# Optimization experiments

Hardware: AMD Instinct MI355X
Metric: run time of the kernel (lower is better)

Reference implementation:

```python
import jax, jax.numpy as jnp
import numpy as np

B, L, D, H = 4, 2048, 256, 512


def silu_backward(x):
    s = jax.nn.silu(x)
    return s + jax.nn.sigmoid(x) * (1.0 - s)


def setup_inputs() -> dict:
    key = jax.random.key(0)
    ks = jax.random.split(key, 12)
    sc = 0.02
    return {
        "x": jax.random.normal(ks[0], (B, L, D), jnp.float32),
        "W1": jax.random.normal(ks[1], (B, H, D), jnp.float32) * sc,
        "W2": jax.random.normal(ks[2], (B, D, H), jnp.float32) * sc,
        "Wq": jax.random.normal(ks[3], (D, D), jnp.float32) * sc,
        "bq": jnp.zeros((D,), jnp.float32),
        "Wk": jax.random.normal(ks[4], (D, D), jnp.float32) * sc,
        "bk": jnp.zeros((D,), jnp.float32),
        "Wv": jax.random.normal(ks[5], (D, D), jnp.float32) * sc,
        "bv": jnp.zeros((D,), jnp.float32),
        "w_lr": jax.random.normal(ks[6], (D,), jnp.float32) * sc,
        "b_lr": jnp.zeros((), jnp.float32),
        "w_wd": jax.random.normal(ks[7], (D,), jnp.float32) * sc,
        "b_wd": jnp.zeros((), jnp.float32),
        "log_base_lr": jnp.asarray(np.log(0.1), jnp.float32),
        "log_base_wd": jnp.asarray(np.log(0.5), jnp.float32),
    }


def reference(x, W1, W2, Wq, bq, Wk, bk, Wv, bv, w_lr, b_lr, w_wd, b_wd, log_base_lr, log_base_wd):
    b, l, d = x.shape
    query = x @ Wq + bq
    key = x @ Wk + bk
    value = x @ Wv + bv
    lr = jnp.exp(log_base_lr) * jax.nn.sigmoid(x @ w_lr + b_lr)          # [b,l]
    log_wd = jnp.log(1.0 - jnp.exp(log_base_wd) * jax.nn.sigmoid(x @ w_wd + b_wd))  # [b,l]

    wd_cross = jnp.exp(jnp.cumsum(log_wd, axis=1))                       # [b,l]
    idx = jnp.arange(l)
    strict_upper = idx[:, None] < idx[None, :]                           # (m, j): j > m
    A = jnp.where(strict_upper[None], log_wd[:, None, :], 0.0)           # [b,m,j]
    wd_inner = jnp.exp(jnp.cumsum(A, axis=2)) * (idx[:, None] <= idx[None, :])[None]  # [b,m,j]

    X1 = key
    Z1 = jnp.einsum('bhd,bld->blh', W1, X1)
    X2 = jax.nn.silu(Z1)
    Z2 = jnp.einsum('bdh,blh->bld', W2, X2)
    grad_Z2 = Z2 - value
    grad_X2 = jnp.einsum('bdh,bld->blh', W2, grad_Z2)
    grad_Z1 = silu_backward(Z1) * grad_X2

    X1_ = query
    mask_X1X1_ = jnp.einsum('bld,bmd->blm', X1, X1_) * wd_inner
    Z1_inner = -jnp.einsum('blh,bl,blm->bmh', grad_Z1, lr, mask_X1X1_)
    Z1_cross = jnp.einsum('bhd,bld,bl->blh', W1, X1_, wd_cross)
    Z1_ = Z1_inner + Z1_cross

    W1_next = (-jnp.einsum('blh,bl,bld->bhd', grad_Z1, lr * wd_inner[:, :, -1], X1)
               + W1 * wd_cross[:, -1][:, None, None])

    X2_ = jax.nn.silu(Z1_)
    mask_X2X2_ = jnp.einsum('blh,bmh->blm', X2, X2_) * wd_inner
    Z2_inner = -jnp.einsum('bld,bl,blm->bmd', grad_Z2, lr, mask_X2X2_)
    Z2_cross = jnp.einsum('bdh,blh,bl->bld', W2, X2_, wd_cross)
    Z2_ = Z2_inner + Z2_cross

    W2_next = (-jnp.einsum('bld,bl,blh->bdh', grad_Z2, lr * wd_inner[:, :, -1], X2)
               + W2 * wd_cross[:, -1][:, None, None])

    return (Z2_, W1_next, W2_next)
```

## Files before the change

kernel.cpp:

```cpp
#include <hip/hip_runtime.h>

typedef __bf16 bf16;
typedef __bf16 bf16x8 __attribute__((ext_vector_type(8)));
typedef __bf16 bf16x4 __attribute__((ext_vector_type(4)));
typedef float  f32x4  __attribute__((ext_vector_type(4)));

#define SB 72
#define CUTOFF -18.0

__device__ __forceinline__ float silu_f(float x){
  float s = 1.f/(1.f+__expf(-x));
  return x*s;
}
__device__ __forceinline__ float silu_bwd_f(float x){
  float s = 1.f/(1.f+__expf(-x));
  float si = x*s;
  return si + s*(1.f-si);
}

struct MArgs {
  const bf16* A; const bf16* B;
  long sA, sB;
  int lda, ldb;
  int M, N, K;
  int mode;
  float* Cf; long sCf;
  bf16*  Cb; long sCb;
  bf16*  Cb2; long sCb2;
  bf16*  Ct;  long sCt;  int ldct;
  bf16*  Ct2; long sCt2;
  int ldc;
  const float* auxf; int ldax; long sAuxf;
  const bf16*  auxb; long sAuxb;
  const float* rowv; long sRowv;
  const float* rowv2; long sRowv2;
  const double* cd;  long sCd;
  const float* clp;  long sClp;
  bf16* Q; bf16* Ko; float* Vo; const float* bqkv;
};

template<int TM>
__device__ __forceinline__ void gemm_body(const MArgs& g, int bm, int bn, int bz)
{
  constexpr int TTP = (TM==64) ? 72 : 136;
  constexpr int BUF = (TM+64)*SB;
  __shared__ __align__(16) bf16 sh[2*BUF];

  const int row0 = bm*TM, col0 = bn*64;
  constexpr int NI  = TM/32;
  constexpr int TPR = 256/TM;
  constexpr int EPR = 64/TPR;
  constexpr int NCH = EPR/8;

  const bf16* A = g.A + (long)bz*g.sA;
  const bf16* B = g.B + (long)bz*g.sB;
  const double* cd = g.cd ? g.cd + (long)bz*g.sCd : (const double*)0;
  float* Cf = g.Cf ? g.Cf + (long)bz*g.sCf : (float*)0;
  bf16* Cb  = g.Cb ? g.Cb + (long)bz*g.sCb : (bf16*)0;
  bf16* Cb2 = g.Cb2 ? g.Cb2 + (long)bz*g.sCb2 : (bf16*)0;
  bf16* Ct  = g.Ct ? g.Ct + (long)bz*g.sCt : (bf16*)0;
  bf16* Ct2 = g.Ct2 ? g.Ct2 + (long)bz*g.sCt2 : (bf16*)0;
  const float* auxf = g.auxf ? g.auxf + (long)bz*g.sAuxf : (const float*)0;
  const bf16*  auxb = g.auxb ? g.auxb + (long)bz*g.sAuxb : (const bf16*)0;
  const float* rowv = g.rowv ? g.rowv + (long)bz*g.sRowv : (const float*)0;
  const float* rowv2 = g.rowv2 ? g.rowv2 + (long)bz*g.sRowv2 : (const float*)0;

  const int tid = threadIdx.x;
  const int mode = g.mode;
  const int lane = tid & 63;
  const int w = tid >> 6;
  const int wr = (w >> 1) * (TM/2), wc = (w & 1) * 32;
  const int l15 = lane & 15;
  const int quad = lane >> 4;

  f32x4 acc[NI][2];
  #pragma unroll
  for (int i=0;i<NI;i++)
    #pragma unroll
    for (int j=0;j<2;j++)
      #pragma unroll
      for (int r=0;r<4;r++) acc[i][j][r] = 0.f;

  const int rowA = tid / TPR, kA = (tid % TPR) * EPR;
  const int rowB = tid >> 2,  kB = (tid & 3) * 16;

  int klo = 0;
  if (cd && mode == 10) {
    const double cref = cd[g.K-1];
    const int nch = g.K >> 6;
    bool dead = (lane < nch-1) && ((cref - cd[lane*64+63]) < CUTOFF);
    unsigned long long mask = __ballot(dead);
    klo = (int)__builtin_ctzll(~mask) * 64;
  }

  const bf16* Abase = A + (long)(row0+rowA)*g.lda + kA;
  const bf16* Bbase = B + (long)(col0+rowB)*g.ldb + kB;

  bf16x8 paA[NCH], pbA0, pbA1, paB[NCH], pbB0, pbB1;
  #pragma unroll
  for (int p=0;p<NCH;p++) paA[p] = *(const bf16x8*)(Abase + klo + p*8);
  pbA0 = *(const bf16x8*)(Bbase + klo);
  pbA1 = *(const bf16x8*)(Bbase + klo + 8);
  if (klo + 64 < g.K) {
    #pragma unroll
    for (int p=0;p<NCH;p++) paB[p] = *(const bf16x8*)(Abase + klo + 64 + p*8);
    pbB0 = *(const bf16x8*)(Bbase + klo + 64);
    pbB1 = *(const bf16x8*)(Bbase + klo + 64 + 8);
  }

  auto compute = [&](const bf16* As, const bf16* Bs){
    #pragma unroll
    for (int ch=0; ch<2; ch++){
      bf16x8 af[NI], bf2[2];
      #pragma unroll
      for (int i=0;i<NI;i++) af[i]  = *(const bf16x8*)&As[(wr + i*16 + l15)*SB + ch*32 + quad*8];
      #pragma unroll
      for (int j=0;j<2;j++) bf2[j] = *(const bf16x8*)&Bs[(wc + j*16 + l15)*SB + ch*32 + quad*8];
      #pragma unroll
      for (int i=0;i<NI;i++)
        #pragma unroll
        for (int j=0;j<2;j++)
          acc[i][j] = __builtin_amdgcn_mfma_f32_16x16x32_bf16(af[i], bf2[j], acc[i][j], 0, 0, 0);
    }
  };

  for (int k0 = klo; k0 < g.K; k0 += 128) {
    {
      bf16* As = sh; bf16* Bs = sh + TM*SB;
      #pragma unroll
      for (int p=0;p<NCH;p++) *(bf16x8*)&As[rowA*SB + kA + p*8] = paA[p];
      *(bf16x8*)&Bs[rowB*SB + kB]     = pbA0;
      *(bf16x8*)&Bs[rowB*SB + kB + 8] = pbA1;
      __syncthreads();
      if (k0 + 128 < g.K) {
        #pragma unroll
        for (int p=0;p<NCH;p++) paA[p] = *(const bf16x8*)(Abase + k0 + 128 + p*8);
        pbA0 = *(const bf16x8*)(Bbase + k0 + 128);
        pbA1 = *(const bf16x8*)(Bbase + k0 + 128 + 8);
      }
      compute(As, Bs);
    }
    if (k0 + 64 < g.K) {
      bf16* As = sh + BUF; bf16* Bs = sh + BUF + TM*SB;
      #pragma unroll
      for (int p=0;p<NCH;p++) *(bf16x8*)&As[rowA*SB + kA + p*8] = paB[p];
      *(bf16x8*)&Bs[rowB*SB + kB]     = pbB0;
      *(bf16x8*)&Bs[rowB*SB + kB + 8] = pbB1;
      __syncthreads();
      if (k0 + 192 < g.K) {
        #pragma unroll
        for (int p=0;p<NCH;p++) paB[p] = *(const bf16x8*)(Abase + k0 + 192 + p*8);
        pbB0 = *(const bf16x8*)(Bbase + k0 + 192);
        pbB1 = *(const bf16x8*)(Bbase + k0 + 192 + 8);
      }
      compute(As, Bs);
    }
  }

  float clv = 0.f;
  if (mode == 10) clv = *(g.clp + (long)bz*g.sClp);

  bf16* Pt12 = (bf16*)0; int slotl0 = 0;
  if (mode == 12) {
    const int d = (row0 & ~127) - col0;
    const int slot = (d + 64) >> 7;
    slotl0 = (row0 & ~127) - slot*128;
    Pt12 = Cb + ((long)bm*3 + slot) * (64*128);
  }

  const bool hasT = (TM==64) ? (mode==1 || mode==2 || mode==3)
                             : (mode==11 && col0 >= 256 && col0 < 512);

  #pragma unroll
  for (int i=0;i<NI;i++){
    const int rb = row0 + wr + i*16 + quad*4;
    const int rloc = wr + i*16 + quad*4;
    #pragma unroll
    for (int j=0;j<2;j++){
      const int c = col0 + wc + j*16 + l15;
      const int cloc = wc + j*16 + l15;
      bf16 tv[4], tv2[4]; bool doT = false, doT2 = false;
      #pragma unroll
      for (int reg=0; reg<4; reg++){
        const int r = rb + reg;
        float v = acc[i][j][reg];
        const long co = (long)r*g.ldc + c;
        switch (mode) {
          case 1: {
            Cb[co]  = (bf16)v;
            float sv = silu_f(v);
            Cb2[co] = (bf16)sv;
            tv[reg] = (bf16)(sv * rowv[r]); doT = true;
          } break;
          case 2: {
            bf16 o = (bf16)(v - auxf[(long)r*g.ldax + c]);
            Cb[co] = o; tv[reg] = o; doT = true;
          } break;
          case 3: {
            float v3 = silu_bwd_f((float)auxb[(long)r*g.ldax + c]) * v * rowv[r];
            tv[reg]  = (bf16)v3;
            tv2[reg] = (bf16)(v3 * rowv2[r]);
            doT = true; doT2 = true;
          } break;
          case 10: {
            Cf[co] = v + auxf[(long)r*g.ldax + c]*clv;
          } break;
          case 11: {
            float o = v + g.bqkv[c];
            if (c < 256)      g.Q [(long)r*256 + c]       = (bf16)o;
            else if (c < 512) { g.Ko[(long)r*256 + (c-256)] = (bf16)o; tv[reg] = (bf16)o; doT = true; }
            else              g.Vo[(long)r*256 + (c-512)] = o;
          } break;
          case 12: {
            const float cm = (float)cd[r];
            const float cl = (float)cd[c];
            float pv = -v * __expf(cm - cl);
            if (rowv) pv *= rowv[c];
            if (c > r) pv = 0.f;
            Pt12[(r - row0)*128 + (c - slotl0)] = (bf16)pv;
          } break;
        }
      }
      if (hasT && doT) {
        bf16x4 t4 = { tv[0], tv[1], tv[2], tv[3] };
        *(bf16x4*)&sh[cloc*TTP + rloc] = t4;
        if (doT2) {
          bf16x4 t4b = { tv2[0], tv2[1], tv2[2], tv2[3] };
          *(bf16x4*)&sh[64*72 + cloc*TTP + rloc] = t4b;
        }
      }
    }
  }

  if (hasT) {
    __syncthreads();
    if constexpr (TM == 64) {
      const int cl = tid >> 2, rl = (tid & 3)*16;
      bf16x8 u0 = *(const bf16x8*)&sh[cl*72 + rl];
      bf16x8 u1 = *(const bf16x8*)&sh[cl*72 + rl + 8];
      bf16* d = Ct + (long)(col0+cl)*g.ldct + row0 + rl;
      *(bf16x8*)d       = u0;
      *(bf16x8*)(d + 8) = u1;
      if (mode == 3) {
        bf16x8 v0 = *(const bf16x8*)&sh[64*72 + cl*72 + rl];
        bf16x8 v1 = *(const bf16x8*)&sh[64*72 + cl*72 + rl + 8];
        bf16* d2 = Ct2 + (long)(col0+cl)*g.ldct + row0 + rl;
        *(bf16x8*)d2       = v0;
        *(bf16x8*)(d2 + 8) = v1;
      }
    } else {
      const int cl = tid >> 2, rl = (tid & 3)*32;
      const int b = row0 / g.ldct, l0r = row0 % g.ldct;
      bf16* d = Ct + (long)b*g.sCt + (long)(col0-256+cl)*g.ldct + l0r + rl;
      #pragma unroll
      for (int p=0;p<4;p++)
        *(bf16x8*)(d + p*8) = *(const bf16x8*)&sh[cl*136 + rl + p*8];
    }
  }
}

__device__ __forceinline__ bool pgen_prep(const MArgs& g, int mt, int hs, int bz, int& bnOut)
{
  const int slot = hs >> 1, half = hs & 1;
  const int m0 = mt*64;
  const int l0 = (m0 & ~127) - slot*128;
  if (l0 < 0) return false;
  const double* cd = g.cd + (long)bz*g.sCd;
  const int lref = (l0+127 < m0) ? (l0+127) : m0;
  if (cd[m0] - cd[lref] < CUTOFF) return false;
  const int l0h = l0 + half*64;
  if (l0h > m0) {
    bf16* Pt = g.Cb + (long)bz*g.sCb + ((long)mt*3 + slot) * (64*128);
    const int row = threadIdx.x >> 2, colb = 64 + (threadIdx.x & 3)*16;
    bf16x8 z;
    #pragma unroll
    for (int q=0;q<8;q++) z[q] = (bf16)0.f;
    *(bf16x8*)&Pt[row*128 + colb]     = z;
    *(bf16x8*)&Pt[row*128 + colb + 8] = z;
    return false;
  }
  bnOut = l0h >> 6;
  return true;
}

__global__ __launch_bounds__(256)
void mfma_gemm64(MArgs g){ gemm_body<64>(g, blockIdx.x, blockIdx.y, blockIdx.z); }

struct CumArgs {
  const float* lw; const float* lr;
  double* cd; float* wdc; float* se1; float* se2; int L;
};

__device__ __forceinline__ void cumsum_body(const CumArgs& a, int b)
{
  __shared__ double sum_s[256];
  const int t = threadIdx.x;
  const int L = a.L;
  const float* lwb = a.lw + (long)b*L;
  double loc[8];
  double s = 0.0;
  #pragma unroll
  for (int i=0;i<8;i++){ s += (double)lwb[t*8+i]; loc[i] = s; }
  sum_s[t] = s;
  __syncthreads();
  for (int off=1; off<256; off<<=1){
    double v = 0.0;
    if (t >= off) v = sum_s[t-off];
    __syncthreads();
    sum_s[t] += v;
    __syncthreads();
  }
  const double prefix = (t > 0) ? sum_s[t-1] : 0.0;
  const double total  = sum_s[255];
  #pragma unroll
  for (int i=0;i<8;i++){
    double c = prefix + loc[i];
    long idx = (long)b*L + t*8 + i;
    a.cd[idx]  = c;
    a.wdc[idx] = (float)exp(c);
    double e = exp(total - c);
    a.se1[idx] = (float)(-e);
    a.se2[idx] = (float)(-e) * a.lr[idx];
  }
}


__global__ __launch_bounds__(256)
void qkv_cum(MArgs g, CumArgs c)
{
  if (blockIdx.x == 64) {
    if (blockIdx.y < 4) cumsum_body(c, blockIdx.y);
    return;
  }
  gemm_body<128>(g, blockIdx.x, blockIdx.y, 0);
}

__global__ __launch_bounds__(256)
void gz2p1(MArgs gz, MArgs p1)
{
  const int bid = blockIdx.x;
  if (bid < 512) {
    gemm_body<64>(gz, bid & 31, (bid >> 5) & 3, bid >> 7);
    return;
  }
  const int i = bid - 512;
  const int mt = i & 31, q = i >> 5;
  const int hs = q % 6, bz = q / 6;
  int bn;
  if (pgen_prep(p1, mt, hs, bz, bn))
    gemm_body<64>(p1, mt, bn, bz);
}

__global__ __launch_bounds__(256)
void p2wn(MArgs p2, MArgs w1n, MArgs w2n)
{
  const int bid = blockIdx.x;
  if (bid < 768) {
    const int mt = bid & 31, q = bid >> 5;
    const int hs = q % 6, bz = q / 6;
    int bn;
    if (pgen_prep(p2, mt, hs, bz, bn))
      gemm_body<64>(p2, mt, bn, bz);
    return;
  }
  const int i = bid - 768;
  if (i < 128) {
    gemm_body<64>(w1n, i & 7, (i >> 3) & 3, i >> 5);
    return;
  }
  const int j = i - 128;
  gemm_body<64>(w2n, j & 3, (j >> 2) & 7, j >> 5);
}

struct CArgs {
  const bf16 *A, *W, *P, *B2;
  long sA, sW, sB2;
  int ldb2;
  const double* cd; long sCd;
  const float* wdc; long sWdc;
  float* Cf; long sCf;
  bf16* Cb; long sCb;
  int ldc;
};

template<int KS64, int SILU, int ZSPLIT>
__global__ __launch_bounds__(256)
void cons(CArgs g)
{
  const int mt = blockIdx.x;
  const int m0 = mt*64, n0 = blockIdx.y*64;
  const int bz   = ZSPLIT ? (blockIdx.z >> 1) : blockIdx.z;
  const int half = ZSPLIT ? (blockIdx.z & 1)  : 0;
  const int K1 = KS64*64;
  const bf16* A  = g.A  + (long)bz*g.sA;
  const bf16* W  = g.W  + (long)bz*g.sW;
  const bf16* B2 = g.B2 + (long)bz*g.sB2;
  const double* cd = g.cd + (long)bz*g.sCd;
  const float* wdc = g.wdc + (long)bz*g.sWdc;

  const int tid = threadIdx.x;
  const int lane = tid & 63, w = tid >> 6;
  const int wr = (w>>1)*32, wc = (w&1)*32;
  const int l15 = lane & 15, quad = lane >> 4;
  const int rowA = tid >> 2, kA = (tid & 3) * 16;

  bool alive[3];
  int nalive = 0;
  #pragma unroll
  for (int s=0;s<3;s++){
    const int l0 = (m0 & ~127) - s*128;
    bool a = (l0 >= 0);
    if (a) {
      const int lref = (l0+127 < m0) ? (l0+127) : m0;
      a = (cd[m0] - cd[lref] >= CUTOFF);
    }
    alive[s] = a; nalive += a ? 1 : 0;
  }
  if (ZSPLIT && half == 1 && nalive == 0) return;

  constexpr int BUFC = 128*SB;
  __shared__ __align__(16) bf16 sh[2*BUFC];

  f32x4 O[2][2];
  #pragma unroll
  for (int i=0;i<2;i++)
    #pragma unroll
    for (int j=0;j<2;j++)
      #pragma unroll
      for (int r=0;r<4;r++) O[i][j][r] = 0.f;

  auto compute = [&](const bf16* As, const bf16* Bs){
    #pragma unroll
    for (int ch=0; ch<2; ch++){
      bf16x8 af[2], bfr[2];
      #pragma unroll
      for (int i=0;i<2;i++) af[i]  = *(const bf16x8*)&As[(wr + i*16 + l15)*SB + ch*32 + quad*8];
      #pragma unroll
      for (int j=0;j<2;j++) bfr[j] = *(const bf16x8*)&Bs[(wc + j*16 + l15)*SB + ch*32 + quad*8];
      #pragma unroll
      for (int i=0;i<2;i++)
        #pragma unroll
        for (int j=0;j<2;j++)
          O[i][j] = __builtin_amdgcn_mfma_f32_16x16x32_bf16(af[i], bfr[j], O[i][j], 0, 0, 0);
    }
  };

  if (half == 0) {
    const bf16* Abase = A + (long)(m0+rowA)*K1 + kA;
    const bf16* Wbase = W + (long)(n0+rowA)*K1 + kA;
    bf16x8 aA0,aA1,wA0,wA1, aB0,aB1,wB0,wB1;
    aA0 = *(const bf16x8*)Abase;        aA1 = *(const bf16x8*)(Abase + 8);
    wA0 = *(const bf16x8*)Wbase;        wA1 = *(const bf16x8*)(Wbase + 8);
    aB0 = *(const bf16x8*)(Abase + 64); aB1 = *(const bf16x8*)(Abase + 72);
    wB0 = *(const bf16x8*)(Wbase + 64); wB1 = *(const bf16x8*)(Wbase + 72);
    for (int ks=0; ks<KS64; ks+=2){
      {
        bf16* As = sh; bf16* Bs = sh + 64*SB;
        *(bf16x8*)&As[rowA*SB + kA]     = aA0;
        *(bf16x8*)&As[rowA*SB + kA + 8] = aA1;
        *(bf16x8*)&Bs[rowA*SB + kA]     = wA0;
        *(bf16x8*)&Bs[rowA*SB + kA + 8] = wA1;
        __syncthreads();
        if (ks+2 < KS64) {
          const int kn = (ks+2)*64;
          aA0 = *(const bf16x8*)(Abase + kn); aA1 = *(const bf16x8*)(Abase + kn + 8);
          wA0 = *(const bf16x8*)(Wbase + kn); wA1 = *(const bf16x8*)(Wbase + kn + 8);
        }
        compute(As, Bs);
      }
      {
        bf16* As = sh + BUFC; bf16* Bs = sh + BUFC + 64*SB;
        *(bf16x8*)&As[rowA*SB + kA]     = aB0;
        *(bf16x8*)&As[rowA*SB + kA + 8] = aB1;
        *(bf16x8*)&Bs[rowA*SB + kA]     = wB0;
        *(bf16x8*)&Bs[rowA*SB + kA + 8] = wB1;
        __syncthreads();
        if (ks+3 < KS64) {
          const int kn = (ks+3)*64;
          aB0 = *(const bf16x8*)(Abase + kn); aB1 = *(const bf16x8*)(Abase + kn + 8);
          wB0 = *(const bf16x8*)(Wbase + kn); wB1 = *(const bf16x8*)(Wbase + kn + 8);
        }
        compute(As, Bs);
      }
    }
    #pragma unroll
    for (int i=0;i<2;i++)
      #pragma unroll
      for (int reg=0; reg<4; reg++){
        const float s = wdc[m0 + wr + i*16 + quad*4 + reg];
        #pragma unroll
        for (int j=0;j<2;j++) O[i][j][reg] *= s;
      }
  }

  if (!ZSPLIT || half == 1) {
    int s0a=0, s1a=0, s2a=0, na=0;
    #pragma unroll
    for (int s=0;s<3;s++) if (alive[s]) { if (na==0) s0a=s; else if (na==1) s1a=s; else s2a=s; na++; }
    const int nst = na*2;
    if (nst > 0) {
      auto Pptr = [&](int t)->const bf16* {
        const int i = t>>1;
        const int s = (i==0) ? s0a : ((i==1) ? s1a : s2a);
        return g.P + (((long)bz*32 + mt)*3 + s)*(64*128) + (long)rowA*128 + (t&1)*64 + kA;
      };
      auto Bptr = [&](int t)->const bf16* {
        const int i = t>>1;
        const int s = (i==0) ? s0a : ((i==1) ? s1a : s2a);
        const int l0 = (m0 & ~127) - s*128;
        return B2 + (long)(n0+rowA)*g.ldb2 + l0 + (t&1)*64 + kA;
      };
      bf16x8 pA0,pA1,bA0,bA1, pB0,pB1,bB0,bB1;
      { const bf16* pp = Pptr(0); pA0 = *(const bf16x8*)pp; pA1 = *(const bf16x8*)(pp+8);
        const bf16* bb = Bptr(0); bA0 = *(const bf16x8*)bb; bA1 = *(const bf16x8*)(bb+8); }
      { const bf16* pp = Pptr(1); pB0 = *(const bf16x8*)pp; pB1 = *(const bf16x8*)(pp+8);
        const bf16* bb = Bptr(1); bB0 = *(const bf16x8*)bb; bB1 = *(const bf16x8*)(bb+8); }
      for (int t=0; t<nst; t+=2){
        {
          bf16* As = sh; bf16* Bs = sh + 64*SB;
          *(bf16x8*)&As[rowA*SB + kA]     = pA0;
          *(bf16x8*)&As[rowA*SB + kA + 8] = pA1;
          *(bf16x8*)&Bs[rowA*SB + kA]     = bA0;
          *(bf16x8*)&Bs[rowA*SB + kA + 8] = bA1;
          __syncthreads();
          if (t+2 < nst) {
            const bf16* pp = Pptr(t+2); pA0 = *(const bf16x8*)pp; pA1 = *(const bf16x8*)(pp+8);
            const bf16* bb = Bptr(t+2); bA0 = *(const bf16x8*)bb; bA1 = *(const bf16x8*)(bb+8);
          }
          compute(As, Bs);
        }
        {
          bf16* As = sh + BUFC; bf16* Bs = sh + BUFC + 64*SB;
          *(bf16x8*)&As[rowA*SB + kA]     = pB0;
          *(bf16x8*)&As[rowA*SB + kA + 8] = pB1;
          *(bf16x8*)&Bs[rowA*SB + kA]     = bB0;
          *(bf16x8*)&Bs[rowA*SB + kA + 8] = bB1;
          __syncthreads();
          if (t+3 < nst) {
            const bf16* pp = Pptr(t+3); pB0 = *(const bf16x8*)pp; pB1 = *(const bf16x8*)(pp+8);
            const bf16* bb = Bptr(t+3); bB0 = *(const bf16x8*)bb; bB1 = *(const bf16x8*)(bb+8);
          }
          compute(As, Bs);
        }
      }
    }
  }

  #pragma unroll
  for (int i=0;i<2;i++){
    const int rb = m0 + wr + i*16 + quad*4;
    #pragma unroll
    for (int j=0;j<2;j++){
      const int c = n0 + wc + j*16 + l15;
      #pragma unroll
      for (int reg=0; reg<4; reg++){
        const long co = (long)(rb+reg)*g.ldc + c;
        if (ZSPLIT)     unsafeAtomicAdd(&g.Cf[(long)bz*g.sCf + co], O[i][j][reg]);
        else if (SILU)  g.Cb[(long)bz*g.sCb + co] = (bf16)silu_f(O[i][j][reg]);
        else            g.Cf[(long)bz*g.sCf + co] = O[i][j][reg];
      }
    }
  }
}

struct FrontArgs {
  const float *x, *W1, *W2, *Wq, *Wk, *Wv;
  bf16 *xb, *W1b, *W2b, *Wqkvt, *W2t;
  float* out0;
  const float *wlr, *blr, *wwd, *bwd, *lbl, *lbw;
  float *lr, *lw;
  const float *bq, *bk, *bv; float* bqkv;
  long LD4, HD4, HD;
};

__global__ __launch_bounds__(256)
void front_kernel(FrontArgs f)
{
  __shared__ bf16 t[64][72];
  const int bid = blockIdx.x;
  const int tid = threadIdx.x;

  if (bid < 1536) {
    const float* src; bf16* dst; long n; long base;
    if (bid < 1024)      { src = f.x;  dst = f.xb;  n = f.LD4; base = (long)bid*2048; }
    else if (bid < 1280) { src = f.W1; dst = f.W1b; n = f.HD4; base = (long)(bid-1024)*2048; }
    else                 { src = f.W2; dst = f.W2b; n = f.HD4; base = (long)(bid-1280)*2048; }
    long i = base + (long)tid*8;
    if (i >= n) return;
    float4 a = *(const float4*)&src[i];
    float4 b = *(const float4*)&src[i+4];
    bf16x8 o;
    o[0]=(bf16)a.x; o[1]=(bf16)a.y; o[2]=(bf16)a.z; o[3]=(bf16)a.w;
    o[4]=(bf16)b.x; o[5]=(bf16)b.y; o[6]=(bf16)b.z; o[7]=(bf16)b.w;
    *(bf16x8*)&dst[i] = o;
    return;
  }
  if (bid < 2560) {
    long i = (long)(bid-1536)*2048 + (long)tid*8;
    float4 z = {0.f,0.f,0.f,0.f};
    *(float4*)&f.out0[i]   = z;
    *(float4*)&f.out0[i+4] = z;
    return;
  }
  if (bid < 2736) {
    const float* ip; bf16* op; int R, C; int r0, c0;
    if (bid < 2608) {
      const int r = bid - 2560;
      const int z = r >> 4, rem = r & 15;
      ip = z==0 ? f.Wq : (z==1 ? f.Wk : f.Wv);
      op = f.Wqkvt + (long)z*256*256;
      R = 256; C = 256;
      r0 = (rem & 3)*64; c0 = (rem >> 2)*64;
    } else {
      const int r = bid - 2608;
      const int b = r >> 5, rem = r & 31;
      ip = f.W2 + (long)b*f.HD;
      op = f.W2t + (long)b*f.HD;
      R = 256; C = 512;
      r0 = (rem & 3)*64; c0 = (rem >> 2)*64;
    }
    const int lr_ = tid>>2, lc = (tid&3)*16;
    #pragma unroll
    for (int q=0;q<4;q++){
      float4 a = *(const float4*)&ip[(long)(r0+lr_)*C + c0+lc + q*4];
      t[lr_][lc+q*4+0] = (bf16)a.x; t[lr_][lc+q*4+1] = (bf16)a.y;
      t[lr_][lc+q*4+2] = (bf16)a.z; t[lr_][lc+q*4+3] = (bf16)a.w;
    }
    __syncthreads();
    const int oc = tid>>2, orr = (tid&3)*16;
    bf16x8 u, v;
    #pragma unroll
    for (int i=0;i<8;i++){ u[i] = t[orr+i][oc]; v[i] = t[orr+8+i][oc]; }
    *(bf16x8*)&op[(long)(c0+oc)*R + r0+orr]   = u;
    *(bf16x8*)&op[(long)(c0+oc)*R + r0+orr+8] = v;
    return;
  }
  if (bid < 4784) {
    const int row  = (bid-2736)*4 + (tid >> 6);
    const int lane = tid & 63;
    const float4 a = ((const float4*)(f.x + (long)row*256))[lane];
    const float4 u = ((const float4*)f.wlr)[lane];
    const float4 w = ((const float4*)f.wwd)[lane];
    float d1 = a.x*u.x + a.y*u.y + a.z*u.z + a.w*u.w;
    float d2 = a.x*w.x + a.y*w.y + a.z*w.z + a.w*w.w;
    #pragma unroll
    for (int off=32; off; off>>=1) {
      d1 += __shfl_down(d1, off);
      d2 += __shfl_down(d2, off);
    }
    if (lane == 0) {
      float s1 = 1.f/(1.f+expf(-(d1 + f.blr[0])));
      f.lr[row] = expf(f.lbl[0]) * s1;
      float s2 = 1.f/(1.f+expf(-(d2 + f.bwd[0])));
      f.lw[row] = logf(1.f - expf(f.lbw[0]) * s2);
    }
    return;
  }
  for (int i = tid; i < 768; i += 256)
    f.bqkv[i] = (i<256) ? f.bq[i] : ((i<512) ? f.bk[i-256] : f.bv[i-512]);
}

extern "C" void kernel_launch(void* const* d_in, const int* in_sizes, int n_in,
                              void* d_out, int out_size, void* d_ws, size_t ws_size,
                              hipStream_t stream)
{
  const int Bn = 4, L = 2048, D = 256, H = 512;
  const long LD = (long)L*D, LH = (long)L*H, HD = (long)H*D;

  const float* x   = (const float*)d_in[0];
  const float* W1  = (const float*)d_in[1];
  const float* W2  = (const float*)d_in[2];
  const float* Wq  = (const float*)d_in[3];
  const float* bq  = (const float*)d_in[4];
  const float* Wk  = (const float*)d_in[5];
  const float* bk  = (const float*)d_in[6];
  const float* Wv  = (const float*)d_in[7];
  const float* bv  = (const float*)d_in[8];
  const float* wlr = (const float*)d_in[9];
  const float* blr = (const float*)d_in[10];
  const float* wwd = (const float*)d_in[11];
  const float* bwd = (const float*)d_in[12];
  const float* lbl = (const float*)d_in[13];
  const float* lbw = (const float*)d_in[14];
  (void)in_sizes; (void)n_in; (void)out_size; (void)ws_size;

  float* out0 = (float*)d_out;
  float* out1 = out0 + (long)Bn*LD;
  float* out2 = out1 + (long)Bn*HD;

  char* wsp = (char*)d_ws;
  size_t off = 0;
  auto alloc = [&](size_t bytes)->void*{
    void* p = wsp + off; off += (bytes + 255) & ~(size_t)255; return p;
  };
  bf16* xb    = (bf16*)alloc((size_t)Bn*LD*2);
  bf16* Wqkvt = (bf16*)alloc((size_t)3*D*D*2);
  float* bqkv = (float*)alloc((size_t)3*D*4);
  bf16* W1b  = (bf16*)alloc((size_t)Bn*HD*2);
  bf16* W2b  = (bf16*)alloc((size_t)Bn*HD*2);
  bf16* W2t  = (bf16*)alloc((size_t)Bn*HD*2);
  bf16* Qb   = (bf16*)alloc((size_t)Bn*LD*2);
  bf16* Kb   = (bf16*)alloc((size_t)Bn*LD*2);
  bf16* Kt   = (bf16*)alloc((size_t)Bn*LD*2);
  float* Vf  = (float*)alloc((size_t)Bn*LD*4);
  bf16* Z1b  = (bf16*)alloc((size_t)Bn*LH*2);
  bf16* X2b  = (bf16*)alloc((size_t)Bn*LH*2);
  bf16* X2t  = (bf16*)alloc((size_t)Bn*LH*2);
  bf16* gZb  = (bf16*)alloc((size_t)Bn*LD*2);
  bf16* gZt  = (bf16*)alloc((size_t)Bn*LD*2);
  bf16* A1t  = (bf16*)alloc((size_t)Bn*LH*2);
  bf16* A1s  = (bf16*)alloc((size_t)Bn*LH*2);
  bf16* X2_b = (bf16*)alloc((size_t)Bn*LH*2);
  bf16* Pb1  = (bf16*)alloc((size_t)Bn*32*3*64*128*2);
  bf16* Pb2  = (bf16*)alloc((size_t)Bn*32*3*64*128*2);
  float* lrb = (float*)alloc((size_t)Bn*L*4);
  float* lwb = (float*)alloc((size_t)Bn*L*4);
  float* wdc = (float*)alloc((size_t)Bn*L*4);
  float* se1 = (float*)alloc((size_t)Bn*L*4);
  float* se2 = (float*)alloc((size_t)Bn*L*4);
  double* cdb = (double*)alloc((size_t)Bn*L*8);

  const long sP = (long)32*3*64*128;

  {
    FrontArgs f{};
    f.x = x; f.W1 = W1; f.W2 = W2; f.Wq = Wq; f.Wk = Wk; f.Wv = Wv;
    f.xb = xb; f.W1b = W1b; f.W2b = W2b; f.Wqkvt = Wqkvt; f.W2t = W2t;
    f.out0 = out0;
    f.wlr = wlr; f.blr = blr; f.wwd = wwd; f.bwd = bwd; f.lbl = lbl; f.lbw = lbw;
    f.lr = lrb; f.lw = lwb;
    f.bq = bq; f.bk = bk; f.bv = bv; f.bqkv = bqkv;
    f.LD4 = Bn*LD; f.HD4 = Bn*HD; f.HD = HD;
    front_kernel<<<dim3(4785), 256, 0, stream>>>(f);
  }
  {
    MArgs g{}; g.A = xb; g.lda = D; g.B = Wqkvt; g.ldb = D;
    g.M = Bn*L; g.N = 3*D; g.K = D; g.mode = 11; g.ldc = 0;
    g.Q = Qb; g.Ko = Kb; g.Vo = Vf; g.bqkv = bqkv;
    g.Ct = Kt; g.sCt = LD; g.ldct = L;
    CumArgs ca{ lwb, lrb, cdb, wdc, se1, se2, L };
    qkv_cum<<<dim3(65, 12), 256, 0, stream>>>(g, ca);
  }
  {
    MArgs g{}; g.A = Kb; g.lda = D; g.sA = LD; g.B = W1b; g.ldb = D; g.sB = HD;
    g.M = L; g.N = H; g.K = D; g.mode = 1; g.ldc = H;
    g.Cb = Z1b; g.sCb = LH; g.Cb2 = X2b; g.sCb2 = LH;
    g.Ct = X2t; g.sCt = LH; g.ldct = L;
    g.rowv = se2; g.sRowv = L;
    mfma_gemm64<<<dim3(32, 8, 4), 256, 0, stream>>>(g);
  }
  {
    MArgs gz{}; gz.A = X2b; gz.lda = H; gz.sA = LH; gz.B = W2b; gz.ldb = H; gz.sB = HD;
    gz.M = L; gz.N = D; gz.K = H; gz.mode = 2; gz.ldc = D;
    gz.auxf = Vf; gz.ldax = D; gz.sAuxf = LD; gz.Cb = gZb; gz.sCb = LD;
    gz.Ct = gZt; gz.sCt = LD; gz.ldct = L;

    MArgs p1{}; p1.A = Qb; p1.lda = D; p1.sA = LD; p1.B = Kb; p1.ldb = D; p1.sB = LD;
    p1.K = D; p1.mode = 12; p1.ldc = 0;
    p1.Cb = Pb1; p1.sCb = sP;
    p1.cd = cdb; p1.sCd = L;

    gz2p1<<<dim3(512 + 768), 256, 0, stream>>>(gz, p1);
  }
  {
    MArgs g{}; g.A = gZb; g.lda = D; g.sA = LD; g.B = W2t; g.ldb = D; g.sB = HD;
    g.M = L; g.N = H; g.K = D; g.mode = 3; g.ldc = H;
    g.auxb = Z1b; g.ldax = H; g.sAuxb = LH;
    g.rowv = lrb; g.sRowv = L; g.rowv2 = se1; g.sRowv2 = L;
    g.Ct = A1t; g.sCt = LH; g.ldct = L;
    g.Ct2 = A1s; g.sCt2 = LH;
    mfma_gemm64<<<dim3(32, 8, 4), 256, 0, stream>>>(g);
  }
  {
    CArgs c{};
    c.A = Qb; c.sA = LD; c.W = W1b; c.sW = HD;
    c.P = Pb1; c.B2 = A1t; c.sB2 = LH; c.ldb2 = L;
    c.cd = cdb; c.sCd = L; c.wdc = wdc; c.sWdc = L;
    c.Cb = X2_b; c.sCb = LH; c.ldc = H;
    cons<4,1,0><<<dim3(32, H/64, Bn), 256, 0, stream>>>(c);
  }
  {
    MArgs p2{}; p2.A = X2_b; p2.lda = H; p2.sA = LH; p2.B = X2b; p2.ldb = H; p2.sB = LH;
    p2.K = H; p2.mode = 12; p2.ldc = 0;
    p2.Cb = Pb2; p2.sCb = sP;
    p2.cd = cdb; p2.sCd = L;
    p2.rowv = lrb; p2.sRowv = L;

    MArgs g1{}; g1.A = A1s; g1.lda = L; g1.sA = LH; g1.B = Kt; g1.ldb = L; g1.sB = LD;
    g1.M = H; g1.N = D; g1.K = L; g1.mode = 10; g1.ldc = D;
    g1.cd = cdb; g1.sCd = L;
    g1.auxf = W1; g1.ldax = D; g1.sAuxf = HD; g1.clp = wdc + (L-1); g1.sClp = L;
    g1.Cf = out1; g1.sCf = HD;

    MArgs g2{}; g2.A = gZt; g2.lda = L; g2.sA = LD; g2.B = X2t; g2.ldb = L; g2.sB = LH;
    g2.M = D; g2.N = H; g2.K = L; g2.mode = 10; g2.ldc = H;
    g2.cd = cdb; g2.sCd = L;
    g2.auxf = W2; g2.ldax = H; g2.sAuxf = HD; g2.clp = wdc + (L-1); g2.sClp = L;
    g2.Cf = out2; g2.sCf = HD;

    p2wn<<<dim3(768 + 128 + 128), 256, 0, stream>>>(p2, g1, g2);
  }
  {
    CArgs c{};
    c.A = X2_b; c.sA = LH; c.W = W2b; c.sW = HD;
    c.P = Pb2; c.B2 = gZt; c.sB2 = LD; c.ldb2 = L;
    c.cd = cdb; c.sCd = L; c.wdc = wdc; c.sWdc = L;
    c.Cf = out0; c.sCf = LD; c.ldc = D;
    cons<8,0,1><<<dim3(32, D/64, Bn*2), 256, 0, stream>>>(c);
  }
}
```

Baseline: 255.4 us.

## Split fused multi-role kernels into separate launches and move cumsum to own kernel

Undoes the horizontal fusion of several stages: the cumsum moves out of the QKV kernel into its own small kernel (which also packs the biases), the QKV GEMM switches from 128-row to 64-row tiles, the gZ2/P1 and P2/W-next fused grids become separate launches, and the W1/W2-next GEMMs run last in a combined 3D grid. This simplifies scheduling and removes branch-divergent block roles, but adds kernel launches and serialization and loses the overlap between independent stages.

```diff
diff --git a/kernel.cpp b/kernel.cpp
--- a/kernel.cpp
+++ b/kernel.cpp
@@ -42,7 +42,6 @@
 template<int TM>
 __device__ __forceinline__ void gemm_body(const MArgs& g, int bm, int bn, int bz)
 {
-  constexpr int TTP = (TM==64) ? 72 : 136;
   constexpr int BUF = (TM+64)*SB;
   __shared__ __align__(16) bf16 sh[2*BUF];
 
@@ -168,8 +167,8 @@
     Pt12 = Cb + ((long)bm*3 + slot) * (64*128);
   }
 
-  const bool hasT = (TM==64) ? (mode==1 || mode==2 || mode==3)
-                             : (mode==11 && col0 >= 256 && col0 < 512);
+  const bool hasT = (mode==1 || mode==2 || mode==3) ||
+                    (mode==11 && col0 >= 256 && col0 < 512);
 
   #pragma unroll
   for (int i=0;i<NI;i++){
@@ -223,10 +222,10 @@
       }
       if (hasT && doT) {
         bf16x4 t4 = { tv[0], tv[1], tv[2], tv[3] };
-        *(bf16x4*)&sh[cloc*TTP + rloc] = t4;
+        *(bf16x4*)&sh[cloc*72 + rloc] = t4;
         if (doT2) {
           bf16x4 t4b = { tv2[0], tv2[1], tv2[2], tv2[3] };
-          *(bf16x4*)&sh[64*72 + cloc*TTP + rloc] = t4b;
+          *(bf16x4*)&sh[64*72 + cloc*72 + rloc] = t4b;
         }
       }
     }
@@ -234,29 +233,38 @@
 
   if (hasT) {
     __syncthreads();
-    if constexpr (TM == 64) {
-      const int cl = tid >> 2, rl = (tid & 3)*16;
-      bf16x8 u0 = *(const bf16x8*)&sh[cl*72 + rl];
-      bf16x8 u1 = *(const bf16x8*)&sh[cl*72 + rl + 8];
-      bf16* d = Ct + (long)(col0+cl)*g.ldct + row0 + rl;
-      *(bf16x8*)d       = u0;
-      *(bf16x8*)(d + 8) = u1;
-      if (mode == 3) {
-        bf16x8 v0 = *(const bf16x8*)&sh[64*72 + cl*72 + rl];
-        bf16x8 v1 = *(const bf16x8*)&sh[64*72 + cl*72 + rl + 8];
-        bf16* d2 = Ct2 + (long)(col0+cl)*g.ldct + row0 + rl;
-        *(bf16x8*)d2       = v0;
-        *(bf16x8*)(d2 + 8) = v1;
-      }
+    const int cl = tid >> 2, rl = (tid & 3)*16;
+    bf16x8 u0 = *(const bf16x8*)&sh[cl*72 + rl];
+    bf16x8 u1 = *(const bf16x8*)&sh[cl*72 + rl + 8];
+    bf16* d;
+    if (mode == 11) {
+      const int b = row0 >> 11, l0r = row0 & 2047;
+      d = Ct + (long)b*g.sCt + (long)(col0-256+cl)*g.ldct + l0r + rl;
     } else {
-      const int cl = tid >> 2, rl = (tid & 3)*32;
-      const int b = row0 / g.ldct, l0r = row0 % g.ldct;
-      bf16* d = Ct + (long)b*g.sCt + (long)(col0-256+cl)*g.ldct + l0r + rl;
-      #pragma unroll
-      for (int p=0;p<4;p++)
-        *(bf16x8*)(d + p*8) = *(const bf16x8*)&sh[cl*136 + rl + p*8];
-    }
-  }
+      d = Ct + (long)(col0+cl)*g.ldct + row0 + rl;
+    }
+    *(bf16x8*)d       = u0;
+    *(bf16x8*)(d + 8) = u1;
+    if (mode == 3) {
+      bf16x8 v0 = *(const bf16x8*)&sh[64*72 + cl*72 + rl];
+      bf16x8 v1 = *(const bf16x8*)&sh[64*72 + cl*72 + rl + 8];
+      bf16* d2 = Ct2 + (long)(col0+cl)*g.ldct + row0 + rl;
+      *(bf16x8*)d2       = v0;
+      *(bf16x8*)(d2 + 8) = v1;
+    }
+  }
+}
+
+__global__ __launch_bounds__(256)
+void mfma_gemm64(MArgs g){ gemm_body<64>(g, blockIdx.x, blockIdx.y, blockIdx.z); }
+
+__global__ __launch_bounds__(256)
+void wnext_gemm(MArgs g1, MArgs g2){
+  const int z = blockIdx.z;
+  const MArgs& g = (z < 4) ? g1 : g2;
+  const int bz = z & 3;
+  if ((int)blockIdx.x*64 >= g.M || (int)blockIdx.y*64 >= g.N) return;
+  gemm_body<64>(g, blockIdx.x, blockIdx.y, bz);
 }
 
 __device__ __forceinline__ bool pgen_prep(const MArgs& g, int mt, int hs, int bz, int& bnOut)
@@ -284,92 +292,10 @@
 }
 
 __global__ __launch_bounds__(256)
-void mfma_gemm64(MArgs g){ gemm_body<64>(g, blockIdx.x, blockIdx.y, blockIdx.z); }
-
-struct CumArgs {
-  const float* lw; const float* lr;
-  double* cd; float* wdc; float* se1; float* se2; int L;
-};
-
-__device__ __forceinline__ void cumsum_body(const CumArgs& a, int b)
-{
-  __shared__ double sum_s[256];
-  const int t = threadIdx.x;
-  const int L = a.L;
-  const float* lwb = a.lw + (long)b*L;
-  double loc[8];
-  double s = 0.0;
-  #pragma unroll
-  for (int i=0;i<8;i++){ s += (double)lwb[t*8+i]; loc[i] = s; }
-  sum_s[t] = s;
-  __syncthreads();
-  for (int off=1; off<256; off<<=1){
-    double v = 0.0;
-    if (t >= off) v = sum_s[t-off];
-    __syncthreads();
-    sum_s[t] += v;
-    __syncthreads();
-  }
-  const double prefix = (t > 0) ? sum_s[t-1] : 0.0;
-  const double total  = sum_s[255];
-  #pragma unroll
-  for (int i=0;i<8;i++){
-    double c = prefix + loc[i];
-    long idx = (long)b*L + t*8 + i;
-    a.cd[idx]  = c;
-    a.wdc[idx] = (float)exp(c);
-    double e = exp(total - c);
-    a.se1[idx] = (float)(-e);
-    a.se2[idx] = (float)(-e) * a.lr[idx];
-  }
-}
-
-
-__global__ __launch_bounds__(256)
-void qkv_cum(MArgs g, CumArgs c)
-{
-  if (blockIdx.x == 64) {
-    if (blockIdx.y < 4) cumsum_body(c, blockIdx.y);
-    return;
-  }
-  gemm_body<128>(g, blockIdx.x, blockIdx.y, 0);
-}
-
-__global__ __launch_bounds__(256)
-void gz2p1(MArgs gz, MArgs p1)
-{
-  const int bid = blockIdx.x;
-  if (bid < 512) {
-    gemm_body<64>(gz, bid & 31, (bid >> 5) & 3, bid >> 7);
-    return;
-  }
-  const int i = bid - 512;
-  const int mt = i & 31, q = i >> 5;
-  const int hs = q % 6, bz = q / 6;
+void pgen64(MArgs g){
   int bn;
-  if (pgen_prep(p1, mt, hs, bz, bn))
-    gemm_body<64>(p1, mt, bn, bz);
-}
-
-__global__ __launch_bounds__(256)
-void p2wn(MArgs p2, MArgs w1n, MArgs w2n)
-{
-  const int bid = blockIdx.x;
-  if (bid < 768) {
-    const int mt = bid & 31, q = bid >> 5;
-    const int hs = q % 6, bz = q / 6;
-    int bn;
-    if (pgen_prep(p2, mt, hs, bz, bn))
-      gemm_body<64>(p2, mt, bn, bz);
-    return;
-  }
-  const int i = bid - 768;
-  if (i < 128) {
-    gemm_body<64>(w1n, i & 7, (i >> 3) & 3, i >> 5);
-    return;
-  }
-  const int j = i - 128;
-  gemm_body<64>(w2n, j & 3, (j >> 2) & 7, j >> 5);
+  if (pgen_prep(g, blockIdx.x, blockIdx.y, blockIdx.z, bn))
+    gemm_body<64>(g, blockIdx.x, bn, blockIdx.z);
 }
 
 struct CArgs {
@@ -569,7 +495,6 @@
   float* out0;
   const float *wlr, *blr, *wwd, *bwd, *lbl, *lbw;
   float *lr, *lw;
-  const float *bq, *bk, *bv; float* bqkv;
   long LD4, HD4, HD;
 };
 
@@ -635,7 +560,7 @@
     *(bf16x8*)&op[(long)(c0+oc)*R + r0+orr+8] = v;
     return;
   }
-  if (bid < 4784) {
+  {
     const int row  = (bid-2736)*4 + (tid >> 6);
     const int lane = tid & 63;
     const float4 a = ((const float4*)(f.x + (long)row*256))[lane];
@@ -654,10 +579,50 @@
       float s2 = 1.f/(1.f+expf(-(d2 + f.bwd[0])));
       f.lw[row] = logf(1.f - expf(f.lbw[0]) * s2);
     }
+  }
+}
+
+__global__ __launch_bounds__(256)
+void cumsum_kernel(const float* __restrict__ lw, const float* __restrict__ lr,
+                   double* __restrict__ cd, float* __restrict__ wdc,
+                   float* __restrict__ se1, float* __restrict__ se2, int L,
+                   const float* __restrict__ bq, const float* __restrict__ bk,
+                   const float* __restrict__ bv, float* __restrict__ bqkv)
+{
+  const int b = blockIdx.x;
+  const int t = threadIdx.x;
+  if (b == 4) {
+    for (int i = t; i < 768; i += 256)
+      bqkv[i] = (i<256) ? bq[i] : ((i<512) ? bk[i-256] : bv[i-512]);
     return;
   }
-  for (int i = tid; i < 768; i += 256)
-    f.bqkv[i] = (i<256) ? f.bq[i] : ((i<512) ? f.bk[i-256] : f.bv[i-512]);
+  const float* lwb = lw + (long)b*L;
+  __shared__ double sum_s[256];
+  double loc[8];
+  double s = 0.0;
+  #pragma unroll
+  for (int i=0;i<8;i++){ s += (double)lwb[t*8+i]; loc[i] = s; }
+  sum_s[t] = s;
+  __syncthreads();
+  for (int off=1; off<256; off<<=1){
+    double v = 0.0;
+    if (t >= off) v = sum_s[t-off];
+    __syncthreads();
+    sum_s[t] += v;
+    __syncthreads();
+  }
+  const double prefix = (t > 0) ? sum_s[t-1] : 0.0;
+  const double total  = sum_s[255];
+  #pragma unroll
+  for (int i=0;i<8;i++){
+    double c = prefix + loc[i];
+    long idx = (long)b*L + t*8 + i;
+    cd[idx]  = c;
+    wdc[idx] = (float)exp(c);
+    double e = exp(total - c);
+    se1[idx] = (float)(-e);
+    se2[idx] = (float)(-e) * lr[idx];
+  }
 }
 
 extern "C" void kernel_launch(void* const* d_in, const int* in_sizes, int n_in,
@@ -722,6 +687,11 @@
 
   const long sP = (long)32*3*64*128;
 
+  auto run64 = [&](const MArgs& g, int Z){
+    dim3 grid(g.M/64, g.N/64, Z);
+    mfma_gemm64<<<grid, 256, 0, stream>>>(g);
+  };
+
   {
     FrontArgs f{};
     f.x = x; f.W1 = W1; f.W2 = W2; f.Wq = Wq; f.Wk = Wk; f.Wv = Wv;
@@ -729,17 +699,17 @@
     f.out0 = out0;
     f.wlr = wlr; f.blr = blr; f.wwd = wwd; f.bwd = bwd; f.lbl = lbl; f.lbw = lbw;
     f.lr = lrb; f.lw = lwb;
-    f.bq = bq; f.bk = bk; f.bv = bv; f.bqkv = bqkv;
     f.LD4 = Bn*LD; f.HD4 = Bn*HD; f.HD = HD;
-    front_kernel<<<dim3(4785), 256, 0, stream>>>(f);
-  }
+    front_kernel<<<dim3(4784), 256, 0, stream>>>(f);
+  }
+  cumsum_kernel<<<dim3(5), 256, 0, stream>>>(lwb, lrb, cdb, wdc, se1, se2, L, bq, bk, bv, bqkv);
+
   {
     MArgs g{}; g.A = xb; g.lda = D; g.B = Wqkvt; g.ldb = D;
     g.M = Bn*L; g.N = 3*D; g.K = D; g.mode = 11; g.ldc = 0;
     g.Q = Qb; g.Ko = Kb; g.Vo = Vf; g.bqkv = bqkv;
     g.Ct = Kt; g.sCt = LD; g.ldct = L;
-    CumArgs ca{ lwb, lrb, cdb, wdc, se1, se2, L };
-    qkv_cum<<<dim3(65, 12), 256, 0, stream>>>(g, ca);
+    mfma_gemm64<<<dim3(128, 12, 1), 256, 0, stream>>>(g);
   }
   {
     MArgs g{}; g.A = Kb; g.lda = D; g.sA = LD; g.B = W1b; g.ldb = D; g.sB = HD;
@@ -747,20 +717,13 @@
     g.Cb = Z1b; g.sCb = LH; g.Cb2 = X2b; g.sCb2 = LH;
     g.Ct = X2t; g.sCt = LH; g.ldct = L;
     g.rowv = se2; g.sRowv = L;
-    mfma_gemm64<<<dim3(32, 8, 4), 256, 0, stream>>>(g);
-  }
-  {
-    MArgs gz{}; gz.A = X2b; gz.lda = H; gz.sA = LH; gz.B = W2b; gz.ldb = H; gz.sB = HD;
-    gz.M = L; gz.N = D; gz.K = H; gz.mode = 2; gz.ldc = D;
-    gz.auxf = Vf; gz.ldax = D; gz.sAuxf = LD; gz.Cb = gZb; gz.sCb = LD;
-    gz.Ct = gZt; gz.sCt = LD; gz.ldct = L;
-
-    MArgs p1{}; p1.A = Qb; p1.lda = D; p1.sA = LD; p1.B = Kb; p1.ldb = D; p1.sB = LD;
-    p1.K = D; p1.mode = 12; p1.ldc = 0;
-    p1.Cb = Pb1; p1.sCb = sP;
-    p1.cd = cdb; p1.sCd = L;
-
-    gz2p1<<<dim3(512 + 768), 256, 0, stream>>>(gz, p1);
+    run64(g, Bn);
+  }
+  {
+    MArgs g{}; g.A = X2b; g.lda = H; g.sA = LH; g.B = W2b; g.ldb = H; g.sB = HD;
+    g.M = L; g.N = D; g.K = H; g.mode = 2; g.ldc = D;
+    g.auxf = Vf; g.ldax = D; g.sAuxf = LD; g.Cb = gZb; g.sCb = LD;
+    g.Ct = gZt; g.sCt = LD; g.ldct = L; run64(g, Bn);
   }
   {
     MArgs g{}; g.A = gZb; g.lda = D; g.sA = LD; g.B = W2t; g.ldb = D; g.sB = HD;
@@ -769,7 +732,14 @@
     g.rowv = lrb; g.sRowv = L; g.rowv2 = se1; g.sRowv2 = L;
     g.Ct = A1t; g.sCt = LH; g.ldct = L;
     g.Ct2 = A1s; g.sCt2 = LH;
-    mfma_gemm64<<<dim3(32, 8, 4), 256, 0, stream>>>(g);
+    run64(g, Bn);
+  }
+  {
+    MArgs p{}; p.A = Qb; p.lda = D; p.sA = LD; p.B = Kb; p.ldb = D; p.sB = LD;
+    p.K = D; p.mode = 12; p.ldc = 0;
+    p.Cb = Pb1; p.sCb = sP;
+    p.cd = cdb; p.sCd = L;
+    pgen64<<<dim3(32, 6, Bn), 256, 0, stream>>>(p);
   }
   {
     CArgs c{};
@@ -780,25 +750,12 @@
     cons<4,1,0><<<dim3(32, H/64, Bn), 256, 0, stream>>>(c);
   }
   {
-    MArgs p2{}; p2.A = X2_b; p2.lda = H; p2.sA = LH; p2.B = X2b; p2.ldb = H; p2.sB = LH;
-    p2.K = H; p2.mode = 12; p2.ldc = 0;
-    p2.Cb = Pb2; p2.sCb = sP;
-    p2.cd = cdb; p2.sCd = L;
-    p2.rowv = lrb; p2.sRowv = L;
-
-    MArgs g1{}; g1.A = A1s; g1.lda = L; g1.sA = LH; g1.B = Kt; g1.ldb = L; g1.sB = LD;
-    g1.M = H; g1.N = D; g1.K = L; g1.mode = 10; g1.ldc = D;
-    g1.cd = cdb; g1.sCd = L;
-    g1.auxf = W1; g1.ldax = D; g1.sAuxf = HD; g1.clp = wdc + (L-1); g1.sClp = L;
-    g1.Cf = out1; g1.sCf = HD;
-
-    MArgs g2{}; g2.A = gZt; g2.lda = L; g2.sA = LD; g2.B = X2t; g2.ldb = L; g2.sB = LH;
-    g2.M = D; g2.N = H; g2.K = L; g2.mode = 10; g2.ldc = H;
-    g2.cd = cdb; g2.sCd = L;
-    g2.auxf = W2; g2.ldax = H; g2.sAuxf = HD; g2.clp = wdc + (L-1); g2.sClp = L;
-    g2.Cf = out2; g2.sCf = HD;
-
-    p2wn<<<dim3(768 + 128 + 128), 256, 0, stream>>>(p2, g1, g2);
+    MArgs p{}; p.A = X2_b; p.lda = H; p.sA = LH; p.B = X2b; p.ldb = H; p.sB = LH;
+    p.K = H; p.mode = 12; p.ldc = 0;
+    p.Cb = Pb2; p.sCb = sP;
+    p.cd = cdb; p.sCd = L;
+    p.rowv = lrb; p.sRowv = L;
+    pgen64<<<dim3(32, 6, Bn), 256, 0, stream>>>(p);
   }
   {
     CArgs c{};
@@ -808,4 +765,19 @@
     c.Cf = out0; c.sCf = LD; c.ldc = D;
     cons<8,0,1><<<dim3(32, D/64, Bn*2), 256, 0, stream>>>(c);
   }
-}
+  {
+    MArgs g1{}; g1.A = A1s; g1.lda = L; g1.sA = LH; g1.B = Kt; g1.ldb = L; g1.sB = LD;
+    g1.M = H; g1.N = D; g1.K = L; g1.mode = 10; g1.ldc = D;
+    g1.cd = cdb; g1.sCd = L;
+    g1.auxf = W1; g1.ldax = D; g1.sAuxf = HD; g1.clp = wdc + (L-1); g1.sClp = L;
+    g1.Cf = out1; g1.sCf = HD;
+
+    MArgs g2{}; g2.A = gZt; g2.lda = L; g2.sA = LD; g2.B = X2t; g2.ldb = L; g2.sB = LH;
+    g2.M = D; g2.N = H; g2.K = L; g2.mode = 10; g2.ldc = H;
+    g2.cd = cdb; g2.sCd = L;
+    g2.auxf = W2; g2.ldax = H; g2.sAuxf = HD; g2.clp = wdc + (L-1); g2.sClp = L;
+    g2.Cf = out2; g2.sCf = HD;
+
+    wnext_gemm<<<dim3(8,8,8), 256, 0, stream>>>(g1, g2);
+  }
+}
```

Result: faster. 222.9 us (-12.7%).
